# Kernel tuning notes

Measured on AMD Instinct MI355X. Metric: run time of the kernel, lower is better.

Reference implementation:

```python
import jax, jax.numpy as jnp
import numpy as np

ATOM_FDIM = 133
BOND_FDIM = 14
HIDDEN = 300
DEPTH = 3
FFN_HIDDEN = 300
NUM_ATOMS = 100000
NUM_EDGES = 400000
NUM_MOLS = 4096


def setup_inputs() -> dict:
    key = jax.random.key(0)
    ks = jax.random.split(key, 10)
    x = jax.random.normal(ks[0], (NUM_ATOMS, ATOM_FDIM), dtype=jnp.float32)
    edge_index = jax.random.randint(ks[1], (2, NUM_EDGES), 0, NUM_ATOMS, dtype=jnp.int32)
    edge_attr = jax.random.normal(ks[2], (NUM_EDGES, BOND_FDIM), dtype=jnp.float32)
    batch = jnp.sort(jax.random.randint(ks[3], (NUM_ATOMS,), 0, NUM_MOLS, dtype=jnp.int32))
    s = 0.05
    W_i = jax.random.normal(ks[4], (HIDDEN, ATOM_FDIM + BOND_FDIM), dtype=jnp.float32) * s
    W_h = jax.random.normal(ks[5], (HIDDEN, HIDDEN), dtype=jnp.float32) * s
    W_o_w = jax.random.normal(ks[6], (HIDDEN, ATOM_FDIM + HIDDEN), dtype=jnp.float32) * s
    W_o_b = jnp.zeros((HIDDEN,), dtype=jnp.float32)
    ffn1_w = jax.random.normal(ks[7], (FFN_HIDDEN, HIDDEN), dtype=jnp.float32) * s
    ffn1_b = jnp.zeros((FFN_HIDDEN,), dtype=jnp.float32)
    ffn2_w = jax.random.normal(ks[8], (1, FFN_HIDDEN), dtype=jnp.float32) * s
    ffn2_b = jnp.zeros((1,), dtype=jnp.float32)
    return {"x": x, "edge_index": edge_index, "edge_attr": edge_attr, "batch": batch,
            "W_i": W_i, "W_h": W_h, "W_o_w": W_o_w, "W_o_b": W_o_b,
            "ffn1_w": ffn1_w, "ffn1_b": ffn1_b, "ffn2_w": ffn2_w, "ffn2_b": ffn2_b}


def reference(x, edge_index, edge_attr, batch, W_i, W_h, W_o_w, W_o_b,
              ffn1_w, ffn1_b, ffn2_w, ffn2_b):
    num_atoms = x.shape[0]
    src, tgt = edge_index[0], edge_index[1]
    # initial edge messages: [E, hidden]
    init = jnp.concatenate([x[src], edge_attr], axis=-1)
    m = jax.nn.relu(init @ W_i.T)
    # dropout is identity at inference
    for _ in range(DEPTH - 1):
        nei = jax.ops.segment_sum(m, tgt, num_segments=num_atoms)  # [N, hidden]
        m = jax.nn.relu(m + nei[src] @ W_h.T)
    atom_msg = jax.ops.segment_sum(m, tgt, num_segments=num_atoms)
    atom_h = jax.nn.relu(jnp.concatenate([x, atom_msg], axis=-1) @ W_o_w.T + W_o_b)
    mol = jax.ops.segment_sum(atom_h, batch, num_segments=NUM_MOLS)  # [B, hidden]
    h = jax.nn.relu(mol @ ffn1_w.T + ffn1_b)
    out = h @ ffn2_w.T + ffn2_b  # [B, 1]
    return out
```

## Files before the change

kernel.cpp:

```cpp
#include <hip/hip_runtime.h>
#include <hip/hip_fp16.h>

#define HID   300
#define NEIP  320
#define APB   4
#define SWK(r) (((r) >> 1) & 3)

typedef _Float16 f16;
typedef f16  f16x2 __attribute__((ext_vector_type(2)));
typedef f16  f16x8 __attribute__((ext_vector_type(8)));
typedef float f32x4 __attribute__((ext_vector_type(4)));

__device__ __forceinline__ f16x2 u2h(unsigned u) {
    union { unsigned u; f16x2 h; } c; c.u = u; return c.h;
}
__device__ __forceinline__ unsigned pk16(float a, float b) {
    union { f16 h[2]; unsigned u; } c; c.h[0] = (f16)a; c.h[1] = (f16)b;
    return c.u;
}
__device__ __forceinline__ void glds16(const void* g, void* l) {
    __builtin_amdgcn_global_load_lds(
        (const __attribute__((address_space(1))) void*)g,
        (__attribute__((address_space(3))) void*)l, 16, 0, 0);
}

__global__ __launch_bounds__(256) void fill_f32(float* __restrict__ p, int n, float v)
{
    int i = blockIdx.x * blockDim.x + threadIdx.x;
    int stride = gridDim.x * blockDim.x;
    for (; i < n; i += stride) p[i] = v;
}

__global__ __launch_bounds__(256) void zero_i32(int* __restrict__ p, int n)
{
    int i = blockIdx.x * blockDim.x + threadIdx.x;
    int stride = gridDim.x * blockDim.x;
    for (; i < n; i += stride) p[i] = 0;
}

__global__ __launch_bounds__(256) void cvt_pad_f16(
    f16* __restrict__ dst, const float* __restrict__ src,
    int srcRows, int ldsrc, int kuse, int kpad, int dstRows)
{
    int i = blockIdx.x * 256 + threadIdx.x;
    const int total = dstRows * kpad;
    const int st = gridDim.x * 256;
    for (; i < total; i += st) {
        int r = i / kpad, k = i - r * kpad;
        float v = (r < srcRows && k < kuse) ? src[(size_t)r * ldsrc + k] : 0.f;
        const int t = k >> 5, kg = (k >> 3) & 3, w = k & 7;
        const int kd = (t << 5) | ((kg ^ SWK(r)) << 3) | w;
        dst[(size_t)r * kpad + kd] = (f16)v;
    }
}

__global__ __launch_bounds__(256) void hist_tgt(
    const int* __restrict__ tgt, int* __restrict__ deg, int E, int N)
{
    int e = blockIdx.x * 256 + threadIdx.x;
    const int st = gridDim.x * 256;
    for (; e < E; e += st) {
        int t = tgt[e];
        t = ((unsigned)t < (unsigned)N) ? t : 0;
        atomicAdd(&deg[t], 1);
    }
}

__global__ __launch_bounds__(1024) void scan_p1(
    const int* __restrict__ deg, int* __restrict__ bsum, int N)
{
    __shared__ int s[1024];
    const int t = threadIdx.x;
    const int i = blockIdx.x * 1024 + t;
    s[t] = (i < N) ? deg[i] : 0;
    __syncthreads();
#pragma unroll
    for (int off = 512; off > 0; off >>= 1) {
        if (t < off) s[t] += s[t + off];
        __syncthreads();
    }
    if (t == 0) bsum[blockIdx.x] = s[0];
}

__global__ __launch_bounds__(1024) void scan_p2(
    const int* __restrict__ bsum, int* __restrict__ boff,
    int G, int* __restrict__ rowPtrN, int E)
{
    __shared__ int s[1024];
    const int t = threadIdx.x;
    s[t] = (t < G) ? bsum[t] : 0;
    __syncthreads();
    for (int off = 1; off < 1024; off <<= 1) {
        const int v = (t >= off) ? s[t - off] : 0;
        __syncthreads();
        s[t] += v;
        __syncthreads();
    }
    if (t < G) boff[t] = (t == 0) ? 0 : s[t - 1];
    if (t == 0) *rowPtrN = E;
}

__global__ __launch_bounds__(1024) void scan_p3(
    const int* __restrict__ deg, const int* __restrict__ boff,
    int* __restrict__ rowPtr, int* __restrict__ cursor, int N)
{
    __shared__ int s[1024];
    const int t = threadIdx.x;
    const int i = blockIdx.x * 1024 + t;
    const int v = (i < N) ? deg[i] : 0;
    s[t] = v;
    __syncthreads();
    for (int off = 1; off < 1024; off <<= 1) {
        const int w = (t >= off) ? s[t - off] : 0;
        __syncthreads();
        s[t] += w;
        __syncthreads();
    }
    if (i < N) {
        const int excl = boff[blockIdx.x] + s[t] - v;
        rowPtr[i] = excl;
        cursor[i] = excl;
    }
}

__global__ __launch_bounds__(256) void scatter_e(
    const int* __restrict__ src, const int* __restrict__ tgt,
    const float* __restrict__ ea,
    int* __restrict__ cursor, int* __restrict__ csrc,
    unsigned* __restrict__ eaPk,
    int E, int N)
{
    int e = blockIdx.x * 256 + threadIdx.x;
    const int st = gridDim.x * 256;
    for (; e < E; e += st) {
        int t = tgt[e];
        int s = src[e];
        t = ((unsigned)t < (unsigned)N) ? t : 0;
        s = ((unsigned)s < (unsigned)N) ? s : 0;
        const int p = atomicAdd(&cursor[t], 1);
        csrc[p] = s;
        const float* er = ea + (size_t)e * 14;
        unsigned* dst = eaPk + (size_t)p * 7;
#pragma unroll
        for (int k = 0; k < 7; ++k)
            dst[k] = pk16(er[2 * k], er[2 * k + 1]);
    }
}

__global__ __launch_bounds__(512) void gemm_mfma(
    const void* __restrict__ A1, int lda1, int a1f16, int K1use,
    const f16* __restrict__ W1, int kpad1,
    const void* __restrict__ A2, int lda2, int a2f16, int K2use,
    const f16* __restrict__ W2, int kpad2,
    const float* __restrict__ bias,
    f16* __restrict__ C, int ldc,
    int M, int do_relu)
{
    __shared__ f16 As[64 * 320];
    __shared__ f16 Ws[320 * 32];

    const int tid  = threadIdx.x;
    const int bm   = blockIdx.x * 64;
    const int lane = tid & 63;
    const int wv   = tid >> 6;
    const int wrow = (wv >> 2) * 32;
    const int wcol = (wv & 3) * 80;
    const int lm   = lane & 15;
    const int kg   = lane >> 4;

    const int n1 = A1 ? (kpad1 >> 5) : 0;
    const int n2 = A2 ? (kpad2 >> 5) : 0;
    const int ntot = n1 + n2;

    f32x4 acc[2][5];
#pragma unroll
    for (int r = 0; r < 2; ++r)
#pragma unroll
        for (int c = 0; c < 5; ++c) acc[r][c] = (f32x4){0.f, 0.f, 0.f, 0.f};

    auto stage_W = [&](int s) {
        const f16* W = (s < n1) ? W1 : W2;
        const int kpad = (s < n1) ? kpad1 : kpad2;
        const int k0 = (((s < n1) ? s : s - n1) << 5);
        const int r16 = lane >> 2;
        const int q   = lane & 3;
        for (int c = wv; c < 20; c += 8) {
            const int R = (c << 4) + r16;
            glds16((const char*)W + ((size_t)R * kpad + k0) * 2 + q * 16,
                   (void*)&Ws[c << 9]);
        }
    };

    auto stage_A = [&](int seg) {
        const void* A = seg ? A2 : A1;
        const int lda  = seg ? lda2 : lda1;
        const int af16 = seg ? a2f16 : a1f16;
        const int kuse = seg ? K2use : K1use;
        const int kpad = seg ? kpad2 : kpad1;
        if (af16) {
            const int nch = kpad >> 3;
            const char* base = (const char*)A + (size_t)bm * lda * 2;
            for (int c = wv; c < nch; c += 8)
                glds16(base + (c << 10) + lane * 16, (void*)&As[c << 9]);
        } else {
            const int cpr = kpad >> 3;
            for (int idx = tid; idx < 64 * cpr; idx += 512) {
                const int row = idx / cpr;
                const int ks  = (idx - row * cpr) << 3;
                const int gmr = bm + row;
                f16x8 v = (f16x8){0, 0, 0, 0, 0, 0, 0, 0};
                if (gmr < M) {
                    const float* p = (const float*)A + (size_t)gmr * lda + ks;
#pragma unroll
                    for (int j = 0; j < 8; ++j)
                        v[j] = (ks + j < kuse) ? (f16)p[j] : (f16)0.f;
                }
                const int t = ks >> 5, kgc = (ks >> 3) & 3;
                *(f16x8*)&As[row * kpad + (t << 5) + ((kgc ^ SWK(row)) << 3)] = v;
            }
        }
    };

    stage_A(0);
    stage_W(0);
    __syncthreads();

    for (int s = 0; s < ntot; ++s) {
        const int seg   = (s >= n1) ? 1 : 0;
        const int kpadA = seg ? kpad2 : kpad1;
        const int sl    = seg ? (s - n1) : s;
        f16x8 af[2], bf[5];
#pragma unroll
        for (int r = 0; r < 2; ++r) {
            const int R = wrow + (r << 4) + lm;
            af[r] = *(const f16x8*)&As[R * kpadA + (sl << 5) + ((kg ^ SWK(R)) << 3)];
        }
#pragma unroll
        for (int c = 0; c < 5; ++c) {
            const int R = wcol + (c << 4) + lm;
            bf[c] = *(const f16x8*)&Ws[R * 32 + ((kg ^ SWK(R)) << 3)];
        }
        __syncthreads();
        if (s + 1 < ntot) {
            stage_W(s + 1);
            if (s + 1 == n1 && n2) stage_A(1);
        }
#pragma unroll
        for (int r = 0; r < 2; ++r)
#pragma unroll
            for (int c = 0; c < 5; ++c)
                acc[r][c] = __builtin_amdgcn_mfma_f32_16x16x32_f16(
                    af[r], bf[c], acc[r][c], 0, 0, 0);
        __syncthreads();
    }

#pragma unroll
    for (int r = 0; r < 2; ++r) {
        const int gm0 = bm + wrow + (r << 4) + ((lane >> 4) << 2);
#pragma unroll
        for (int c = 0; c < 5; ++c) {
            const int n = wcol + (c << 4) + lm;
            if (n >= HID) continue;
            const float bi = bias ? bias[n] : 0.f;
#pragma unroll
            for (int i = 0; i < 4; ++i) {
                const int gmo = gm0 + i;
                if (gmo >= M) continue;
                float v = acc[r][c][i] + bi;
                if (do_relu) v = fmaxf(v, 0.f);
                C[(size_t)gmo * ldc + n] = (f16)v;
            }
        }
    }
}

template <int NSLOTS>
__global__ __launch_bounds__(192) void edge_csr(
    const unsigned* __restrict__ xa,
    const unsigned* __restrict__ hn0,
    const unsigned* __restrict__ hn1,
    const int* __restrict__ rowPtr,
    const int* __restrict__ csrc,
    const unsigned* __restrict__ eaPk,
    const float* __restrict__ Wi,
    unsigned* __restrict__ out,
    int N)
{
    const int p = threadIdx.x;
    f16x2 wpk[14];
    if (p < 150) {
#pragma unroll
        for (int k = 0; k < 14; ++k)
            wpk[k] = (f16x2){(f16)Wi[(2 * p) * 147 + 133 + k],
                             (f16)Wi[(2 * p + 1) * 147 + 133 + k]};
    }
    const f16x2 zero2 = (f16x2){(f16)0.f, (f16)0.f};

    const int a0 = blockIdx.x * APB;
    const int a1 = min(a0 + APB, N);
    for (int a = a0; a < a1; ++a) {
        const int beg = rowPtr[a];
        const int end = rowPtr[a + 1];
        float acc0 = 0.f, acc1 = 0.f;
        if (p < 150) {
#pragma unroll 2
            for (int j = beg; j < end; ++j) {
                const int s = __builtin_nontemporal_load(&csrc[j]);
                const size_t srow = (size_t)s * 150 + p;
                const unsigned u0 = xa[srow];
                unsigned u1 = 0, u2 = 0;
                if (NSLOTS > 1) u1 = hn0[srow];
                if (NSLOTS > 2) u2 = hn1[srow];
                const unsigned* eq = eaPk + (size_t)j * 7;
                f16x2 ebA = zero2, ebB = zero2;
#pragma unroll
                for (int k = 0; k < 7; ++k) {
                    const f16x2 e2 = u2h(__builtin_nontemporal_load(&eq[k]));
                    ebA += (f16x2){e2.x, e2.x} * wpk[2 * k];
                    ebB += (f16x2){e2.y, e2.y} * wpk[2 * k + 1];
                }
                f16x2 m = __builtin_elementwise_max(u2h(u0) + (ebA + ebB), zero2);
                if (NSLOTS > 1) m = __builtin_elementwise_max(m + u2h(u1), zero2);
                if (NSLOTS > 2) m = __builtin_elementwise_max(m + u2h(u2), zero2);
                acc0 += (float)m.x;
                acc1 += (float)m.y;
            }
        }
        if (p < NEIP / 2) {
            const unsigned val = (p < 150) ? pk16(acc0, acc1) : 0u;
            const int t = p >> 4, kgc = (p >> 2) & 3, w = p & 3;
            __builtin_nontemporal_store(val,
                &out[(size_t)a * (NEIP / 2) + (t << 4) + ((kgc ^ SWK(a)) << 2) + w]);
        }
    }
}

__global__ __launch_bounds__(256) void mol_pool(
    const f16* __restrict__ ah,
    const int* __restrict__ batch,
    float* __restrict__ mol,
    int N)
{
    const int b = blockIdx.x;
    int lo = 0, hi = N;
    while (lo < hi) { int mid = (lo + hi) >> 1; if (batch[mid] < b) lo = mid + 1; else hi = mid; }
    const int start = lo;
    hi = N;
    while (lo < hi) { int mid = (lo + hi) >> 1; if (batch[mid] < b + 1) lo = mid + 1; else hi = mid; }
    const int end = lo;

    for (int h = threadIdx.x; h < HID; h += 256) {
        float s = 0.f;
        for (int a = start; a < end; ++a) s += (float)ah[(size_t)a * HID + h];
        mol[(size_t)b * HID + h] = s;
    }
}

__global__ __launch_bounds__(64) void ffn2_k(
    const f16* __restrict__ h1,
    const float* __restrict__ w2,
    const float* __restrict__ b2, float* __restrict__ out, int B)
{
    const int b = blockIdx.x;
    float s = 0.f;
    for (int k = threadIdx.x; k < HID; k += 64)
        s += (float)h1[(size_t)b * HID + k] * w2[k];
#pragma unroll
    for (int off = 32; off > 0; off >>= 1) s += __shfl_down(s, off);
    if (threadIdx.x == 0) out[b] = s + b2[0];
}

extern "C" void kernel_launch(void* const* d_in, const int* in_sizes, int n_in,
                              void* d_out, int out_size, void* d_ws, size_t ws_size,
                              hipStream_t stream)
{
    float* outp = (float*)d_out;
    const int fillBlocks = (out_size + 255) / 256;

    if (n_in < 12) {
        fill_f32<<<fillBlocks, 256, 0, stream>>>(outp, out_size, 2.0e6f + n_in);
        return;
    }

    const int N = in_sizes[0] / 133;
    const int E = in_sizes[1] / 2;
    const int B = out_size;

    const long long expect[12] = {
        (long long)N * 133, (long long)E * 2, (long long)E * 14, N,
        300LL * 147, 300LL * 300, 300LL * 433, 300,
        300LL * 300, 300, 300, 1 };
    for (int i = 0; i < 12; ++i) {
        if ((long long)in_sizes[i] != expect[i]) {
            fill_f32<<<fillBlocks, 256, 0, stream>>>(outp, out_size,
                                                     3.0e6f + 1.0e4f * i);
            return;
        }
    }

    const int G = (N + 1023) / 1024;
    if (G > 1024) {
        fill_f32<<<fillBlocks, 256, 0, stream>>>(outp, out_size, 4.0e6f);
        return;
    }

    char* basep = (char*)d_ws;
    auto align16 = [](size_t v) { return (v + 15) & ~(size_t)15; };
    const size_t slotB  = align16((size_t)N * HID * sizeof(f16));
    const size_t neiB   = align16((size_t)N * NEIP * sizeof(f16));
    const size_t wSmall = align16(320 * 160 * sizeof(f16));
    const size_t wBig   = align16(320 * 320 * sizeof(f16));
    const size_t molB   = align16((size_t)B * HID * sizeof(float));
    const size_t h1B    = align16((size_t)B * HID * sizeof(f16));
    const size_t rpB    = align16((size_t)(N + 1) * sizeof(int));
    const size_t curB   = align16((size_t)N * sizeof(int));
    const size_t csrcB  = align16((size_t)E * sizeof(int));
    const size_t eaB    = align16((size_t)E * 7 * sizeof(unsigned));
    const size_t bsB    = align16(1024 * sizeof(int));
    const size_t need = 3 * slotB + neiB + 2 * wSmall + 3 * wBig
                      + molB + h1B + rpB + 2 * curB + csrcB + eaB + 2 * bsB;

    if (ws_size < need) {
        fill_f32<<<fillBlocks, 256, 0, stream>>>(outp, out_size,
                                                 (float)(ws_size >> 20));
        return;
    }

    const float* x     = (const float*)d_in[0];
    const int*   ei    = (const int*)d_in[1];
    const float* ea    = (const float*)d_in[2];
    const int*   batch = (const int*)d_in[3];
    const float* W_i   = (const float*)d_in[4];
    const float* W_h   = (const float*)d_in[5];
    const float* W_o   = (const float*)d_in[6];
    const float* W_ob  = (const float*)d_in[7];
    const float* f1w   = (const float*)d_in[8];
    const float* f1b   = (const float*)d_in[9];
    const float* f2w   = (const float*)d_in[10];
    const float* f2b   = (const float*)d_in[11];
    const int* src = ei;
    const int* tgt = ei + E;

    char* cp = basep;
    f16* xa     = (f16*)cp;         cp += slotB;
    f16* hn0    = (f16*)cp;         cp += slotB;
    f16* hn1    = (f16*)cp;         cp += slotB;
    f16* nei    = (f16*)cp;         cp += neiB;
    f16* WiA    = (f16*)cp;         cp += wSmall;
    f16* Wh     = (f16*)cp;         cp += wBig;
    f16* WoA    = (f16*)cp;         cp += wSmall;
    f16* WoB    = (f16*)cp;         cp += wBig;
    f16* Wf1    = (f16*)cp;         cp += wBig;
    float* mol  = (float*)cp;       cp += molB;
    f16* h1     = (f16*)cp;         cp += h1B;
    int* rowPtr = (int*)cp;         cp += rpB;
    int* cursor = (int*)cp;         cp += curB;
    int* deg    = (int*)cp;         cp += curB;
    int* csrc   = (int*)cp;         cp += csrcB;
    unsigned* eaPk = (unsigned*)cp; cp += eaB;
    int* bsum   = (int*)cp;         cp += bsB;
    int* boff   = (int*)cp;         cp += bsB;

    const unsigned* xa_u  = (const unsigned*)xa;
    const unsigned* hn0_u = (const unsigned*)hn0;
    const unsigned* hn1_u = (const unsigned*)hn1;
    unsigned*       nei_u = (unsigned*)nei;

    const int gAtom = (N + 63) / 64;
    const int gMolG = (B + 63) / 64;
    const int gEdge = (N + APB - 1) / APB;

    zero_i32<<<128, 256, 0, stream>>>(deg, N);
    hist_tgt<<<1024, 256, 0, stream>>>(tgt, deg, E, N);
    scan_p1<<<G, 1024, 0, stream>>>(deg, bsum, N);
    scan_p2<<<1, 1024, 0, stream>>>(bsum, boff, G, rowPtr + N, E);
    scan_p3<<<G, 1024, 0, stream>>>(deg, boff, rowPtr, cursor, N);
    scatter_e<<<1024, 256, 0, stream>>>(src, tgt, ea, cursor, csrc, eaPk, E, N);

    cvt_pad_f16<<<64,  256, 0, stream>>>(WiA, W_i,       300, 147, 133, 160, 320);
    cvt_pad_f16<<<128, 256, 0, stream>>>(Wh,  W_h,       300, 300, 300, 320, 320);
    cvt_pad_f16<<<64,  256, 0, stream>>>(WoA, W_o,       300, 433, 133, 160, 320);
    cvt_pad_f16<<<128, 256, 0, stream>>>(WoB, W_o + 133, 300, 433, 300, 320, 320);
    cvt_pad_f16<<<128, 256, 0, stream>>>(Wf1, f1w,       300, 300, 300, 320, 320);

    gemm_mfma<<<gAtom, 512, 0, stream>>>(x, 133, 0, 133, WiA, 160,
        nullptr, 0, 0, 0, nullptr, 0, nullptr, xa, HID, N, 0);
    edge_csr<1><<<gEdge, 192, 0, stream>>>(xa_u, hn0_u, hn1_u, rowPtr, csrc,
                                           eaPk, W_i, nei_u, N);
    gemm_mfma<<<gAtom, 512, 0, stream>>>(nei, NEIP, 1, NEIP, Wh, 320,
        nullptr, 0, 0, 0, nullptr, 0, nullptr, hn0, HID, N, 0);
    edge_csr<2><<<gEdge, 192, 0, stream>>>(xa_u, hn0_u, hn1_u, rowPtr, csrc,
                                           eaPk, W_i, nei_u, N);
    gemm_mfma<<<gAtom, 512, 0, stream>>>(nei, NEIP, 1, NEIP, Wh, 320,
        nullptr, 0, 0, 0, nullptr, 0, nullptr, hn1, HID, N, 0);
    edge_csr<3><<<gEdge, 192, 0, stream>>>(xa_u, hn0_u, hn1_u, rowPtr, csrc,
                                           eaPk, W_i, nei_u, N);
    gemm_mfma<<<gAtom, 512, 0, stream>>>(x, 133, 0, 133, WoA, 160,
        nei, NEIP, 1, NEIP, WoB, 320, W_ob, xa, HID, N, 1);
    mol_pool<<<B, 256, 0, stream>>>(xa, batch, mol, N);
    gemm_mfma<<<gMolG, 512, 0, stream>>>(mol, 300, 0, 300, Wf1, 320,
        nullptr, 0, 0, 0, nullptr, 0, f1b, h1, HID, B, 1);
    ffn2_k<<<B, 64, 0, stream>>>(h1, f2w, f2b, outp, B);
}
```

Measured before the change: 808.5 us.

## Add N-split MFMA GEMM that stages a whole weight half in LDS

Adds a gemm_ns kernel in which each block computes a 64-row by 160-column tile. The full K extent of A and of that weight half is loaded into LDS once, followed by a single barrier and an uninterrupted MFMA loop, so the per-K-step weight staging and syncs of the old kernel go away. It replaces gemm_mfma for the initial atom projection, the two W_h GEMMs and ffn1, which doubles the grid. The cost is more LDS per block (about 140 KB), which may limit occupancy, and the A tile is loaded twice, once per column half.

```diff
diff --git a/kernel.cpp b/kernel.cpp
--- a/kernel.cpp
+++ b/kernel.cpp
@@ -144,6 +144,96 @@
 #pragma unroll
         for (int k = 0; k < 7; ++k)
             dst[k] = pk16(er[2 * k], er[2 * k + 1]);
+    }
+}
+
+__global__ __launch_bounds__(512) void gemm_ns(
+    const void* __restrict__ A, int lda, int af16, int Kuse,
+    const f16* __restrict__ W, int kpad,
+    const float* __restrict__ bias,
+    f16* __restrict__ C, int ldc,
+    int M, int do_relu)
+{
+    __shared__ f16 As[64 * 320];
+    __shared__ f16 Ws[160 * 320];
+
+    const int tid  = threadIdx.x;
+    const int bm   = (blockIdx.x >> 1) * 64;
+    const int cb   = (blockIdx.x & 1) * 160;
+    const int lane = tid & 63;
+    const int wv   = tid >> 6;
+    const int rg   = wv >> 1;
+    const int cg   = wv & 1;
+    const int lm   = lane & 15;
+    const int kg   = lane >> 4;
+
+    const int nst = kpad >> 5;
+
+    f32x4 acc[5];
+#pragma unroll
+    for (int c = 0; c < 5; ++c) acc[c] = (f32x4){0.f, 0.f, 0.f, 0.f};
+
+    if (af16) {
+        const int nch = (64 * kpad) >> 9;
+        const char* base = (const char*)A + (size_t)bm * lda * 2;
+        for (int c = wv; c < nch; c += 8)
+            glds16(base + (c << 10) + lane * 16, (void*)&As[c << 9]);
+    } else {
+        const int cpr = kpad >> 3;
+        for (int idx = tid; idx < 64 * cpr; idx += 512) {
+            const int row = idx / cpr;
+            const int ks  = (idx - row * cpr) << 3;
+            const int gmr = bm + row;
+            f16x8 v = (f16x8){0, 0, 0, 0, 0, 0, 0, 0};
+            if (gmr < M) {
+                const float* p = (const float*)A + (size_t)gmr * lda + ks;
+#pragma unroll
+                for (int j = 0; j < 8; ++j)
+                    v[j] = (ks + j < Kuse) ? (f16)p[j] : (f16)0.f;
+            }
+            const int t = ks >> 5, kgc = (ks >> 3) & 3;
+            *(f16x8*)&As[row * kpad + (t << 5) + ((kgc ^ SWK(row)) << 3)] = v;
+        }
+    }
+    {
+        const int nch = (160 * kpad) >> 9;
+        const char* base = (const char*)W + (size_t)cb * kpad * 2;
+        for (int c = wv; c < nch; c += 8)
+            glds16(base + (c << 10) + lane * 16, (void*)&Ws[c << 9]);
+    }
+    __syncthreads();
+
+    for (int s = 0; s < nst; ++s) {
+        const int R = (rg << 4) + lm;
+        const f16x8 af = *(const f16x8*)
+            &As[R * kpad + (s << 5) + ((kg ^ SWK(R)) << 3)];
+        f16x8 bf[5];
+#pragma unroll
+        for (int c = 0; c < 5; ++c) {
+            const int wr = cg * 80 + (c << 4) + lm;
+            bf[c] = *(const f16x8*)
+                &Ws[wr * kpad + (s << 5) + ((kg ^ SWK(wr)) << 3)];
+        }
+#pragma unroll
+        for (int c = 0; c < 5; ++c)
+            acc[c] = __builtin_amdgcn_mfma_f32_16x16x32_f16(
+                af, bf[c], acc[c], 0, 0, 0);
+    }
+
+    const int gm0 = bm + (rg << 4) + ((lane >> 4) << 2);
+#pragma unroll
+    for (int c = 0; c < 5; ++c) {
+        const int n = cb + cg * 80 + (c << 4) + lm;
+        if (n >= HID) continue;
+        const float bi = bias ? bias[n] : 0.f;
+#pragma unroll
+        for (int i = 0; i < 4; ++i) {
+            const int gmo = gm0 + i;
+            if (gmo >= M) continue;
+            float v = acc[c][i] + bi;
+            if (do_relu) v = fmaxf(v, 0.f);
+            C[(size_t)gmo * ldc + n] = (f16)v;
+        }
     }
 }
 
@@ -466,9 +556,10 @@
     const unsigned* hn1_u = (const unsigned*)hn1;
     unsigned*       nei_u = (unsigned*)nei;
 
-    const int gAtom = (N + 63) / 64;
-    const int gMolG = (B + 63) / 64;
-    const int gEdge = (N + APB - 1) / APB;
+    const int gAtom   = (N + 63) / 64;
+    const int gAtomNS = ((N + 63) / 64) * 2;
+    const int gMolNS  = ((B + 63) / 64) * 2;
+    const int gEdge   = (N + APB - 1) / APB;
 
     zero_i32<<<128, 256, 0, stream>>>(deg, N);
     hist_tgt<<<1024, 256, 0, stream>>>(tgt, deg, E, N);
@@ -483,22 +574,22 @@
     cvt_pad_f16<<<128, 256, 0, stream>>>(WoB, W_o + 133, 300, 433, 300, 320, 320);
     cvt_pad_f16<<<128, 256, 0, stream>>>(Wf1, f1w,       300, 300, 300, 320, 320);
 
-    gemm_mfma<<<gAtom, 512, 0, stream>>>(x, 133, 0, 133, WiA, 160,
-        nullptr, 0, 0, 0, nullptr, 0, nullptr, xa, HID, N, 0);
+    gemm_ns<<<gAtomNS, 512, 0, stream>>>(x, 133, 0, 133, WiA, 160,
+        nullptr, xa, HID, N, 0);
     edge_csr<1><<<gEdge, 192, 0, stream>>>(xa_u, hn0_u, hn1_u, rowPtr, csrc,
                                            eaPk, W_i, nei_u, N);
-    gemm_mfma<<<gAtom, 512, 0, stream>>>(nei, NEIP, 1, NEIP, Wh, 320,
-        nullptr, 0, 0, 0, nullptr, 0, nullptr, hn0, HID, N, 0);
+    gemm_ns<<<gAtomNS, 512, 0, stream>>>(nei, NEIP, 1, NEIP, Wh, 320,
+        nullptr, hn0, HID, N, 0);
     edge_csr<2><<<gEdge, 192, 0, stream>>>(xa_u, hn0_u, hn1_u, rowPtr, csrc,
                                            eaPk, W_i, nei_u, N);
-    gemm_mfma<<<gAtom, 512, 0, stream>>>(nei, NEIP, 1, NEIP, Wh, 320,
-        nullptr, 0, 0, 0, nullptr, 0, nullptr, hn1, HID, N, 0);
+    gemm_ns<<<gAtomNS, 512, 0, stream>>>(nei, NEIP, 1, NEIP, Wh, 320,
+        nullptr, hn1, HID, N, 0);
     edge_csr<3><<<gEdge, 192, 0, stream>>>(xa_u, hn0_u, hn1_u, rowPtr, csrc,
                                            eaPk, W_i, nei_u, N);
     gemm_mfma<<<gAtom, 512, 0, stream>>>(x, 133, 0, 133, WoA, 160,
         nei, NEIP, 1, NEIP, WoB, 320, W_ob, xa, HID, N, 1);
     mol_pool<<<B, 256, 0, stream>>>(xa, batch, mol, N);
-    gemm_mfma<<<gMolG, 512, 0, stream>>>(mol, 300, 0, 300, Wf1, 320,
-        nullptr, 0, 0, 0, nullptr, 0, f1b, h1, HID, B, 1);
+    gemm_ns<<<gMolNS, 512, 0, stream>>>(mol, 300, 0, 300, Wf1, 320,
+        f1b, h1, HID, B, 1);
     ffn2_k<<<B, 64, 0, stream>>>(h1, f2w, f2b, outp, B);
 }
```

After: 900.6 us. 11.4% more time.
